# Optimization experiments

Hardware: AMD Instinct MI355X
Metric: run time of the kernel (lower is better)

## Reference

```python
import jax, jax.numpy as jnp
import numpy as np

N = 100000
E = 3200000
K = 4
BN_EPS = 1e-5


def spmm(edge_rows, edge_cols, edge_vals, x):
    # y = A @ x with A in COO: y[r] += v * x[c]
    msgs = edge_vals[:, None] * x[edge_cols]           # [E, d]
    return jax.ops.segment_sum(msgs, edge_rows, num_segments=N)


def setup_inputs() -> dict:
    key = jax.random.key(0)
    ks = jax.random.split(key, 8)
    d_in, d_h, d_out = 256, 256, 64
    return {
        "x": jax.random.normal(ks[0], (N, d_in), jnp.float32),
        "edge_rows": jax.random.randint(ks[1], (E,), 0, N, jnp.int32),
        "edge_cols": jax.random.randint(ks[2], (E,), 0, N, jnp.int32),
        "edge_vals": jax.random.uniform(ks[3], (E,), jnp.float32),
        "bn_gamma": jnp.ones((d_in,), jnp.float32),
        "bn_beta": jnp.zeros((d_in,), jnp.float32),
        "w_in": jax.random.normal(ks[4], (d_in, d_h), jnp.float32) * 0.05,
        "b_in": jnp.zeros((d_h,), jnp.float32),
        "w_conv": jax.random.normal(ks[5], (d_h, d_h), jnp.float32) * 0.05,
        "b_conv": jnp.zeros((d_h,), jnp.float32),
        "w_out": jax.random.normal(ks[6], (d_h, d_out), jnp.float32) * 0.05,
        "b_out": jnp.zeros((d_out,), jnp.float32),
    }


def reference(x, edge_rows, edge_cols, edge_vals, bn_gamma, bn_beta,
              w_in, b_in, w_conv, b_conv, w_out, b_out):
    # BatchNorm1d over node dimension (training-mode batch stats, biased var)
    mean = jnp.mean(x, axis=0)
    var = jnp.var(x, axis=0)
    x = (x - mean) * jax.lax.rsqrt(var + BN_EPS) * bn_gamma + bn_beta
    # in_conv + tanh
    x = jnp.tanh(x @ w_in + b_in)
    # SGConv: k spmm hops then linear, then tanh
    for _ in range(K):
        x = spmm(edge_rows, edge_cols, edge_vals, x)
    x = jnp.tanh(x @ w_conv + b_conv)
    # out_conv (logits)
    return x @ w_out + b_out
```

## Files before the change

### kernel.cpp

```cpp
#include <hip/hip_runtime.h>
#include <hip/hip_fp16.h>

#define NN   100000
#define NNP  100096
#define EE   3200000
#define DD   256
#define DOUTC 64
#define LSTR 40

typedef _Float16 half8 __attribute__((ext_vector_type(8)));
typedef _Float16 half4 __attribute__((ext_vector_type(4)));
typedef float    f32x4 __attribute__((ext_vector_type(4)));

__device__ inline f32x4 mfma16(half8 a, half8 b, f32x4 c) {
    return __builtin_amdgcn_mfma_f32_16x16x32_f16(a, b, c, 0, 0, 0);
}

__global__ void col_stats_kernel(const float* __restrict__ x, float* __restrict__ stats) {
    int t = threadIdx.x;
    int r0 = blockIdx.x * 256;
    int r1 = min(r0 + 256, NN);
    float s = 0.f, s2 = 0.f;
    for (int r = r0; r < r1; ++r) {
        float v = x[(size_t)r * DD + t];
        s += v; s2 += v * v;
    }
    atomicAdd(&stats[t], s);
    atomicAdd(&stats[DD + t], s2);
}

__global__ void fold_bias_kernel(const float* __restrict__ stats,
                                 const float* __restrict__ gamma,
                                 const float* __restrict__ beta,
                                 const float* __restrict__ w_in,
                                 const float* __restrict__ b_in,
                                 float* __restrict__ bfold) {
    __shared__ float sb[DD];
    int t = threadIdx.x;
    float mean = stats[t] * (1.0f / NN);
    float var  = stats[DD + t] * (1.0f / NN) - mean * mean;
    float a = gamma[t] * rsqrtf(var + 1e-5f);
    sb[t] = beta[t] - mean * a;
    __syncthreads();
    float acc = 0.f;
    for (int j = 0; j < DD; ++j) acc += sb[j] * w_in[j * DD + t];
    bfold[t] = b_in[t] + acc;
}

__global__ void split_w1_kernel(const float* __restrict__ stats,
                                const float* __restrict__ gamma,
                                const float* __restrict__ w_in,
                                _Float16* __restrict__ wth, _Float16* __restrict__ wtl) {
    int k = blockIdx.x, n = threadIdx.x;
    float mean = stats[k] * (1.0f / NN);
    float var  = stats[DD + k] * (1.0f / NN) - mean * mean;
    float a = gamma[k] * rsqrtf(var + 1e-5f);
    float v = a * w_in[(size_t)k * DD + n];
    _Float16 hi = (_Float16)v;
    _Float16 lo = (_Float16)(v - (float)hi);
    wth[(size_t)n * DD + k] = hi;
    wtl[(size_t)n * DD + k] = lo;
}

__global__ void split_w_kernel(const float* __restrict__ w, int ncols,
                               _Float16* __restrict__ wth, _Float16* __restrict__ wtl) {
    int k = blockIdx.x, n = threadIdx.x;
    float v = w[(size_t)k * ncols + n];
    _Float16 hi = (_Float16)v;
    _Float16 lo = (_Float16)(v - (float)hi);
    wth[(size_t)n * DD + k] = hi;
    wtl[(size_t)n * DD + k] = lo;
}

__global__ void hist_kernel(const int* __restrict__ rows, int* __restrict__ cnt) {
    int e = blockIdx.x * blockDim.x + threadIdx.x;
    if (e < EE) atomicAdd(&cnt[rows[e]], 1);
}

__global__ void scan1_kernel(const int* __restrict__ in, int* __restrict__ out,
                             int* __restrict__ bsums, int n) {
    __shared__ int s[256];
    int t = threadIdx.x;
    int base = blockIdx.x * 1024;
    int v[4]; int local = 0;
    for (int i = 0; i < 4; ++i) {
        int idx = base + t * 4 + i;
        v[i] = (idx < n) ? in[idx] : 0;
        local += v[i];
    }
    s[t] = local;
    __syncthreads();
    for (int off = 1; off < 256; off <<= 1) {
        int xv = 0;
        if (t >= off) xv = s[t - off];
        __syncthreads();
        if (t >= off) s[t] += xv;
        __syncthreads();
    }
    int excl = s[t] - local;
    if (t == 255) bsums[blockIdx.x] = s[255];
    int run = excl;
    for (int i = 0; i < 4; ++i) {
        int idx = base + t * 4 + i;
        if (idx < n) out[idx] = run;
        run += v[i];
    }
}

__global__ void scan2_kernel(int* __restrict__ bsums, int nb) {
    __shared__ int s[256];
    int t = threadIdx.x;
    int v = (t < nb) ? bsums[t] : 0;
    s[t] = v;
    __syncthreads();
    for (int off = 1; off < 256; off <<= 1) {
        int xv = 0;
        if (t >= off) xv = s[t - off];
        __syncthreads();
        if (t >= off) s[t] += xv;
        __syncthreads();
    }
    if (t < nb) bsums[t] = s[t] - v;
}

__global__ void scan3_kernel(int* __restrict__ out, const int* __restrict__ bsums, int n) {
    int t = threadIdx.x;
    int base = blockIdx.x * 1024;
    int add = bsums[blockIdx.x];
    for (int i = 0; i < 4; ++i) {
        int idx = base + t * 4 + i;
        if (idx < n) out[idx] += add;
    }
    if (blockIdx.x == 0 && t == 0) out[n] = EE;
}

__global__ void scatter_kernel(const int* __restrict__ rows, const int* __restrict__ cols,
                               const float* __restrict__ vals, const int* __restrict__ rp,
                               int* __restrict__ cur, int2* __restrict__ edges) {
    int e = blockIdx.x * blockDim.x + threadIdx.x;
    if (e >= EE) return;
    int r = rows[e];
    int pos = rp[r] + atomicAdd(&cur[r], 1);
    edges[pos] = make_int2(cols[e], __float_as_int(vals[e]));
}

__global__ __launch_bounds__(256) void spmm_kernel(
        const int* __restrict__ rp, const int2* __restrict__ edges,
        const __half* __restrict__ xin, __half* __restrict__ xout) {
    int tid = threadIdx.x;
    int lane = tid & 63;
    int half_id = lane >> 5;
    int sl = lane & 31;
    int r = __builtin_amdgcn_readfirstlane(blockIdx.x * 4 + (tid >> 6));
    int e0 = rp[r], e1 = rp[r + 1];
    const float4* xi = (const float4*)xin;

    float acc[8] = {0.f,0.f,0.f,0.f,0.f,0.f,0.f,0.f};

    int base = e0;
    for (; base + 8 <= e1; base += 8) {
        int2 d[4];
#pragma unroll
        for (int i = 0; i < 4; ++i) d[i] = edges[base + 2*i + half_id];
        float4 xv[4];
#pragma unroll
        for (int i = 0; i < 4; ++i) xv[i] = xi[(size_t)d[i].x * 32 + sl];
#pragma unroll
        for (int i = 0; i < 4; ++i) {
            float v = __int_as_float(d[i].y);
            const __half2* hp = (const __half2*)&xv[i];
            float2 f0 = __half22float2(hp[0]);
            float2 f1 = __half22float2(hp[1]);
            float2 f2 = __half22float2(hp[2]);
            float2 f3 = __half22float2(hp[3]);
            acc[0] += v*f0.x; acc[1] += v*f0.y;
            acc[2] += v*f1.x; acc[3] += v*f1.y;
            acc[4] += v*f2.x; acc[5] += v*f2.y;
            acc[6] += v*f3.x; acc[7] += v*f3.y;
        }
    }
    if (base < e1) {
#pragma unroll
        for (int i = 0; i < 4; ++i) {
            int idx = base + 2*i + half_id;
            bool valid = idx < e1;
            int idxc = valid ? idx : e0;
            int2 d = edges[idxc];
            float v = valid ? __int_as_float(d.y) : 0.f;
            float4 xv = xi[(size_t)d.x * 32 + sl];
            const __half2* hp = (const __half2*)&xv;
            float2 f0 = __half22float2(hp[0]);
            float2 f1 = __half22float2(hp[1]);
            float2 f2 = __half22float2(hp[2]);
            float2 f3 = __half22float2(hp[3]);
            acc[0] += v*f0.x; acc[1] += v*f0.y;
            acc[2] += v*f1.x; acc[3] += v*f1.y;
            acc[4] += v*f2.x; acc[5] += v*f2.y;
            acc[6] += v*f3.x; acc[7] += v*f3.y;
        }
    }
#pragma unroll
    for (int j = 0; j < 8; ++j) acc[j] += __shfl_xor(acc[j], 32, 64);
    if (half_id == 0) {
        union { __half h[8]; float4 f; } u;
#pragma unroll
        for (int j = 0; j < 8; ++j) u.h[j] = __float2half_rn(acc[j]);
        ((float4*)xout)[(size_t)r * 32 + sl] = u.f;
    }
}

template<bool SPLIT_A, bool TANH, typename Tout, int BN>
__global__ __launch_bounds__(256) void gemm_mfma(
    const void* __restrict__ Av, const _Float16* __restrict__ WTh,
    const _Float16* __restrict__ WTl, const float* __restrict__ bias,
    Tout* __restrict__ C, int M_A, int M_C, int NC)
{
    __shared__ _Float16 As_hi[128 * LSTR];
    __shared__ _Float16 As_lo[(SPLIT_A ? 128 : 1) * LSTR];
    __shared__ _Float16 Ws_hi[BN * LSTR];
    __shared__ _Float16 Ws_lo[BN * LSTR];

    int tid = threadIdx.x;
    int lane = tid & 63;
    int w = tid >> 6;
    int q = lane >> 4;
    int r16 = lane & 15;
    int m0 = blockIdx.x * 128;
    int n0 = blockIdx.y * BN;

    constexpr int MT = (BN == 128) ? 4 : 2;
    int wm = (BN == 128) ? (w & 1) * 64 : w * 32;
    int wn = (BN == 128) ? (w >> 1) * 64 : 0;

    f32x4 acc[MT][4];
#pragma unroll
    for (int mt = 0; mt < MT; ++mt)
#pragma unroll
        for (int nt = 0; nt < 4; ++nt) acc[mt][nt] = (f32x4){0.f, 0.f, 0.f, 0.f};

    for (int k0 = 0; k0 < 256; k0 += 32) {
        if (SPLIT_A) {
            const float* A = (const float*)Av;
#pragma unroll
            for (int p = 0; p < 4; ++p) {
                int idx = tid + p * 256;
                int m = idx >> 3, kc = idx & 7;
                int gm = m0 + m;
                float4 av = make_float4(0.f, 0.f, 0.f, 0.f);
                if (gm < M_A) av = *(const float4*)&A[(size_t)gm * 256 + k0 + kc * 4];
                half4 hi, lo;
                hi.x = (_Float16)av.x; lo.x = (_Float16)(av.x - (float)hi.x);
                hi.y = (_Float16)av.y; lo.y = (_Float16)(av.y - (float)hi.y);
                hi.z = (_Float16)av.z; lo.z = (_Float16)(av.z - (float)hi.z);
                hi.w = (_Float16)av.w; lo.w = (_Float16)(av.w - (float)hi.w);
                *(half4*)&As_hi[m * LSTR + kc * 4] = hi;
                *(half4*)&As_lo[m * LSTR + kc * 4] = lo;
            }
        } else {
            const _Float16* A = (const _Float16*)Av;
#pragma unroll
            for (int p = 0; p < 2; ++p) {
                int idx = tid + p * 256;
                int m = idx >> 2, kc = idx & 3;
                half8 av = *(const half8*)&A[(size_t)(m0 + m) * 256 + k0 + kc * 8];
                *(half8*)&As_hi[m * LSTR + kc * 8] = av;
            }
        }
#pragma unroll
        for (int p = 0; p < BN / 64; ++p) {
            int idx = tid + p * 256;
            int n = idx >> 2, kc = idx & 3;
            *(half8*)&Ws_hi[n * LSTR + kc * 8] = *(const half8*)&WTh[(size_t)(n0 + n) * 256 + k0 + kc * 8];
            *(half8*)&Ws_lo[n * LSTR + kc * 8] = *(const half8*)&WTl[(size_t)(n0 + n) * 256 + k0 + kc * 8];
        }
        __syncthreads();

        half8 af_h[MT], af_l[MT], wf_h[4], wf_l[4];
#pragma unroll
        for (int mt = 0; mt < MT; ++mt) {
            int mrow = wm + mt * 16 + r16;
            af_h[mt] = *(const half8*)&As_hi[mrow * LSTR + q * 8];
            if (SPLIT_A) af_l[mt] = *(const half8*)&As_lo[mrow * LSTR + q * 8];
        }
#pragma unroll
        for (int nt = 0; nt < 4; ++nt) {
            int nrow = wn + nt * 16 + r16;
            wf_h[nt] = *(const half8*)&Ws_hi[nrow * LSTR + q * 8];
            wf_l[nt] = *(const half8*)&Ws_lo[nrow * LSTR + q * 8];
        }
#pragma unroll
        for (int mt = 0; mt < MT; ++mt)
#pragma unroll
            for (int nt = 0; nt < 4; ++nt) {
                acc[mt][nt] = mfma16(af_h[mt], wf_h[nt], acc[mt][nt]);
                if (SPLIT_A) acc[mt][nt] = mfma16(af_l[mt], wf_h[nt], acc[mt][nt]);
                acc[mt][nt] = mfma16(af_h[mt], wf_l[nt], acc[mt][nt]);
            }
        __syncthreads();
    }

#pragma unroll
    for (int nt = 0; nt < 4; ++nt) {
        float b = bias[n0 + wn + nt * 16 + r16];
        int gc = n0 + wn + nt * 16 + r16;
#pragma unroll
        for (int mt = 0; mt < MT; ++mt) {
#pragma unroll
            for (int r = 0; r < 4; ++r) {
                int gm = m0 + wm + mt * 16 + q * 4 + r;
                float v = acc[mt][nt][r] + b;
                if (TANH) v = tanhf(v);
                if (gm < M_C) C[(size_t)gm * NC + gc] = (Tout)v;
            }
        }
    }
}

extern "C" void kernel_launch(void* const* d_in, const int* in_sizes, int n_in,
                              void* d_out, int out_size, void* d_ws, size_t ws_size,
                              hipStream_t stream) {
    const float* x      = (const float*)d_in[0];
    const int*   erows  = (const int*)d_in[1];
    const int*   ecols  = (const int*)d_in[2];
    const float* evals  = (const float*)d_in[3];
    const float* gamma  = (const float*)d_in[4];
    const float* beta   = (const float*)d_in[5];
    const float* w_in   = (const float*)d_in[6];
    const float* b_in   = (const float*)d_in[7];
    const float* w_conv = (const float*)d_in[8];
    const float* b_conv = (const float*)d_in[9];
    const float* w_out  = (const float*)d_in[10];
    const float* b_out  = (const float*)d_in[11];
    float* out = (float*)d_out;

    char* ws = (char*)d_ws;
    size_t off = 0;
    auto alloc = [&](size_t bytes) -> void* {
        void* p = ws + off;
        off = (off + bytes + 255) & ~(size_t)255;
        return p;
    };
    _Float16* h1   = (_Float16*)alloc((size_t)NNP * DD * 2);
    _Float16* h2   = (_Float16*)alloc((size_t)NNP * DD * 2);
    int2*  edges = (int2*) alloc((size_t)EE * 8);
    int*   rp    = (int*)  alloc((size_t)(NN + 1) * 4);
    int*   cnt   = (int*)  alloc((size_t)NN * 4);
    int*   cur   = (int*)  alloc((size_t)NN * 4);
    float* stats = (float*)alloc(2 * DD * 4);
    int*   bsums = (int*)  alloc(128 * 4);
    _Float16* wt1h = (_Float16*)alloc((size_t)DD * DD * 2);
    _Float16* wt1l = (_Float16*)alloc((size_t)DD * DD * 2);
    _Float16* wt2h = (_Float16*)alloc((size_t)DD * DD * 2);
    _Float16* wt2l = (_Float16*)alloc((size_t)DD * DD * 2);
    _Float16* wt3h = (_Float16*)alloc((size_t)DOUTC * DD * 2);
    _Float16* wt3l = (_Float16*)alloc((size_t)DOUTC * DD * 2);
    float* bfold = (float*)alloc(DD * 4);

    hipMemsetAsync(cnt,   0, (size_t)NN * 4, stream);
    hipMemsetAsync(cur,   0, (size_t)NN * 4, stream);
    hipMemsetAsync(stats, 0, 2 * DD * 4, stream);

    hist_kernel<<<(EE + 255) / 256, 256, 0, stream>>>(erows, cnt);
    int nb = (NN + 1023) / 1024;
    scan1_kernel<<<nb, 256, 0, stream>>>(cnt, rp, bsums, NN);
    scan2_kernel<<<1, 256, 0, stream>>>(bsums, nb);
    scan3_kernel<<<nb, 256, 0, stream>>>(rp, bsums, NN);
    scatter_kernel<<<(EE + 255) / 256, 256, 0, stream>>>(erows, ecols, evals, rp, cur, edges);

    col_stats_kernel<<<(NN + 255) / 256, 256, 0, stream>>>(x, stats);
    fold_bias_kernel<<<1, 256, 0, stream>>>(stats, gamma, beta, w_in, b_in, bfold);
    split_w1_kernel<<<DD, DD, 0, stream>>>(stats, gamma, w_in, wt1h, wt1l);
    split_w_kernel<<<DD, DD, 0, stream>>>(w_conv, DD, wt2h, wt2l);
    split_w_kernel<<<DD, DOUTC, 0, stream>>>(w_out, DOUTC, wt3h, wt3l);

    dim3 g2(NNP / 128, 2), g1(NNP / 128, 1);
    gemm_mfma<true, true, _Float16, 128><<<g2, 256, 0, stream>>>(
        x, wt1h, wt1l, bfold, h1, NN, NNP, DD);

    spmm_kernel<<<NN / 4, 256, 0, stream>>>(rp, edges, (const __half*)h1, (__half*)h2);
    spmm_kernel<<<NN / 4, 256, 0, stream>>>(rp, edges, (const __half*)h2, (__half*)h1);
    spmm_kernel<<<NN / 4, 256, 0, stream>>>(rp, edges, (const __half*)h1, (__half*)h2);
    spmm_kernel<<<NN / 4, 256, 0, stream>>>(rp, edges, (const __half*)h2, (__half*)h1);

    gemm_mfma<false, true, _Float16, 128><<<g2, 256, 0, stream>>>(
        h1, wt2h, wt2l, b_conv, h2, NNP, NNP, DD);
    gemm_mfma<false, false, float, 64><<<g1, 256, 0, stream>>>(
        h2, wt3h, wt3l, b_out, out, NNP, NN, DOUTC);
}
```

Before: 1.671 ms.

## Split SpMM into two feature-half passes and precompute CSR scatter ranks

Each SpMM hop now runs as two launches, each covering 128 of the 256 fp16 feature columns. Within a launch, four 16-lane groups each gather a different edge, which shrinks the gathered working set per pass so it is more likely to stay in cache. The COO-to-CSR build records each edge's atomic rank during the histogram, so the scatter no longer needs a second atomic pass or its cursor memset. Nontemporal loads and stores are added for edge streams and outputs. In exchange, the edge list is read twice per hop, kernel launches double, and a 12.8MB rank buffer is added.

```diff
diff --git a/kernel.cpp b/kernel.cpp
--- a/kernel.cpp
+++ b/kernel.cpp
@@ -72,9 +72,10 @@
     wtl[(size_t)n * DD + k] = lo;
 }
 
-__global__ void hist_kernel(const int* __restrict__ rows, int* __restrict__ cnt) {
+__global__ void hist_kernel(const int* __restrict__ rows, int* __restrict__ cnt,
+                            int* __restrict__ rank) {
     int e = blockIdx.x * blockDim.x + threadIdx.x;
-    if (e < EE) atomicAdd(&cnt[rows[e]], 1);
+    if (e < EE) rank[e] = atomicAdd(&cnt[rows[e]], 1);
 }
 
 __global__ void scan1_kernel(const int* __restrict__ in, int* __restrict__ out,
@@ -136,58 +137,74 @@
 
 __global__ void scatter_kernel(const int* __restrict__ rows, const int* __restrict__ cols,
                                const float* __restrict__ vals, const int* __restrict__ rp,
-                               int* __restrict__ cur, int2* __restrict__ edges) {
+                               const int* __restrict__ rank, int2* __restrict__ edges) {
     int e = blockIdx.x * blockDim.x + threadIdx.x;
     if (e >= EE) return;
-    int r = rows[e];
-    int pos = rp[r] + atomicAdd(&cur[r], 1);
-    edges[pos] = make_int2(cols[e], __float_as_int(vals[e]));
+    int r = __builtin_nontemporal_load(&rows[e]);
+    int c = __builtin_nontemporal_load(&cols[e]);
+    float v = __builtin_nontemporal_load(&vals[e]);
+    int rk = __builtin_nontemporal_load(&rank[e]);
+    int pos = rp[r] + rk;
+    edges[pos] = make_int2(c, __float_as_int(v));
 }
 
 __global__ __launch_bounds__(256) void spmm_kernel(
         const int* __restrict__ rp, const int2* __restrict__ edges,
-        const __half* __restrict__ xin, __half* __restrict__ xout) {
+        const __half* __restrict__ xin, __half* __restrict__ xout, int ph) {
     int tid = threadIdx.x;
     int lane = tid & 63;
-    int half_id = lane >> 5;
-    int sl = lane & 31;
+    int sub = lane >> 4;
+    int sl = lane & 15;
     int r = __builtin_amdgcn_readfirstlane(blockIdx.x * 4 + (tid >> 6));
     int e0 = rp[r], e1 = rp[r + 1];
     const float4* xi = (const float4*)xin;
+    const long long* epk = (const long long*)edges;
+    int cbase = ph * 16 + sl;
 
     float acc[8] = {0.f,0.f,0.f,0.f,0.f,0.f,0.f,0.f};
 
     int base = e0;
     for (; base + 8 <= e1; base += 8) {
-        int2 d[4];
-#pragma unroll
-        for (int i = 0; i < 4; ++i) d[i] = edges[base + 2*i + half_id];
-        float4 xv[4];
-#pragma unroll
-        for (int i = 0; i < 4; ++i) xv[i] = xi[(size_t)d[i].x * 32 + sl];
-#pragma unroll
-        for (int i = 0; i < 4; ++i) {
-            float v = __int_as_float(d[i].y);
-            const __half2* hp = (const __half2*)&xv[i];
+        long long p0 = __builtin_nontemporal_load(&epk[base + sub]);
+        long long p1 = __builtin_nontemporal_load(&epk[base + 4 + sub]);
+        int c0 = (int)(unsigned int)p0, c1 = (int)(unsigned int)p1;
+        float v0 = __int_as_float((int)(p0 >> 32));
+        float v1 = __int_as_float((int)(p1 >> 32));
+        float4 x0 = xi[(size_t)c0 * 32 + cbase];
+        float4 x1 = xi[(size_t)c1 * 32 + cbase];
+        {
+            const __half2* hp = (const __half2*)&x0;
             float2 f0 = __half22float2(hp[0]);
             float2 f1 = __half22float2(hp[1]);
             float2 f2 = __half22float2(hp[2]);
             float2 f3 = __half22float2(hp[3]);
-            acc[0] += v*f0.x; acc[1] += v*f0.y;
-            acc[2] += v*f1.x; acc[3] += v*f1.y;
-            acc[4] += v*f2.x; acc[5] += v*f2.y;
-            acc[6] += v*f3.x; acc[7] += v*f3.y;
+            acc[0] += v0*f0.x; acc[1] += v0*f0.y;
+            acc[2] += v0*f1.x; acc[3] += v0*f1.y;
+            acc[4] += v0*f2.x; acc[5] += v0*f2.y;
+            acc[6] += v0*f3.x; acc[7] += v0*f3.y;
+        }
+        {
+            const __half2* hp = (const __half2*)&x1;
+            float2 f0 = __half22float2(hp[0]);
+            float2 f1 = __half22float2(hp[1]);
+            float2 f2 = __half22float2(hp[2]);
+            float2 f3 = __half22float2(hp[3]);
+            acc[0] += v1*f0.x; acc[1] += v1*f0.y;
+            acc[2] += v1*f1.x; acc[3] += v1*f1.y;
+            acc[4] += v1*f2.x; acc[5] += v1*f2.y;
+            acc[6] += v1*f3.x; acc[7] += v1*f3.y;
         }
     }
     if (base < e1) {
 #pragma unroll
-        for (int i = 0; i < 4; ++i) {
-            int idx = base + 2*i + half_id;
+        for (int i = 0; i < 2; ++i) {
+            int idx = base + 4*i + sub;
             bool valid = idx < e1;
             int idxc = valid ? idx : e0;
-            int2 d = edges[idxc];
-            float v = valid ? __int_as_float(d.y) : 0.f;
-            float4 xv = xi[(size_t)d.x * 32 + sl];
+            long long p = epk[idxc];
+            int c = (int)(unsigned int)p;
+            float v = valid ? __int_as_float((int)(p >> 32)) : 0.f;
+            float4 xv = xi[(size_t)c * 32 + cbase];
             const __half2* hp = (const __half2*)&xv;
             float2 f0 = __half22float2(hp[0]);
             float2 f1 = __half22float2(hp[1]);
@@ -200,12 +217,15 @@
         }
     }
 #pragma unroll
-    for (int j = 0; j < 8; ++j) acc[j] += __shfl_xor(acc[j], 32, 64);
-    if (half_id == 0) {
-        union { __half h[8]; float4 f; } u;
+    for (int j = 0; j < 8; ++j) {
+        acc[j] += __shfl_xor(acc[j], 16, 64);
+        acc[j] += __shfl_xor(acc[j], 32, 64);
+    }
+    if (sub == 0) {
+        union { __half h[8]; f32x4 f; } u;
 #pragma unroll
         for (int j = 0; j < 8; ++j) u.h[j] = __float2half_rn(acc[j]);
-        ((float4*)xout)[(size_t)r * 32 + sl] = u.f;
+        __builtin_nontemporal_store(u.f, (f32x4*)&((float4*)xout)[(size_t)r * 32 + cbase]);
     }
 }
 
@@ -343,9 +363,9 @@
     _Float16* h1   = (_Float16*)alloc((size_t)NNP * DD * 2);
     _Float16* h2   = (_Float16*)alloc((size_t)NNP * DD * 2);
     int2*  edges = (int2*) alloc((size_t)EE * 8);
+    int*   rank  = (int*)  alloc((size_t)EE * 4);
     int*   rp    = (int*)  alloc((size_t)(NN + 1) * 4);
     int*   cnt   = (int*)  alloc((size_t)NN * 4);
-    int*   cur   = (int*)  alloc((size_t)NN * 4);
     float* stats = (float*)alloc(2 * DD * 4);
     int*   bsums = (int*)  alloc(128 * 4);
     _Float16* wt1h = (_Float16*)alloc((size_t)DD * DD * 2);
@@ -357,15 +377,14 @@
     float* bfold = (float*)alloc(DD * 4);
 
     hipMemsetAsync(cnt,   0, (size_t)NN * 4, stream);
-    hipMemsetAsync(cur,   0, (size_t)NN * 4, stream);
     hipMemsetAsync(stats, 0, 2 * DD * 4, stream);
 
-    hist_kernel<<<(EE + 255) / 256, 256, 0, stream>>>(erows, cnt);
+    hist_kernel<<<(EE + 255) / 256, 256, 0, stream>>>(erows, cnt, rank);
     int nb = (NN + 1023) / 1024;
     scan1_kernel<<<nb, 256, 0, stream>>>(cnt, rp, bsums, NN);
     scan2_kernel<<<1, 256, 0, stream>>>(bsums, nb);
     scan3_kernel<<<nb, 256, 0, stream>>>(rp, bsums, NN);
-    scatter_kernel<<<(EE + 255) / 256, 256, 0, stream>>>(erows, ecols, evals, rp, cur, edges);
+    scatter_kernel<<<(EE + 255) / 256, 256, 0, stream>>>(erows, ecols, evals, rp, rank, edges);
 
     col_stats_kernel<<<(NN + 255) / 256, 256, 0, stream>>>(x, stats);
     fold_bias_kernel<<<1, 256, 0, stream>>>(stats, gamma, beta, w_in, b_in, bfold);
@@ -377,10 +396,14 @@
     gemm_mfma<true, true, _Float16, 128><<<g2, 256, 0, stream>>>(
         x, wt1h, wt1l, bfold, h1, NN, NNP, DD);
 
-    spmm_kernel<<<NN / 4, 256, 0, stream>>>(rp, edges, (const __half*)h1, (__half*)h2);
-    spmm_kernel<<<NN / 4, 256, 0, stream>>>(rp, edges, (const __half*)h2, (__half*)h1);
-    spmm_kernel<<<NN / 4, 256, 0, stream>>>(rp, edges, (const __half*)h1, (__half*)h2);
-    spmm_kernel<<<NN / 4, 256, 0, stream>>>(rp, edges, (const __half*)h2, (__half*)h1);
+    spmm_kernel<<<NN / 4, 256, 0, stream>>>(rp, edges, (const __half*)h1, (__half*)h2, 0);
+    spmm_kernel<<<NN / 4, 256, 0, stream>>>(rp, edges, (const __half*)h1, (__half*)h2, 1);
+    spmm_kernel<<<NN / 4, 256, 0, stream>>>(rp, edges, (const __half*)h2, (__half*)h1, 0);
+    spmm_kernel<<<NN / 4, 256, 0, stream>>>(rp, edges, (const __half*)h2, (__half*)h1, 1);
+    spmm_kernel<<<NN / 4, 256, 0, stream>>>(rp, edges, (const __half*)h1, (__half*)h2, 0);
+    spmm_kernel<<<NN / 4, 256, 0, stream>>>(rp, edges, (const __half*)h1, (__half*)h2, 1);
+    spmm_kernel<<<NN / 4, 256, 0, stream>>>(rp, edges, (const __half*)h2, (__half*)h1, 0);
+    spmm_kernel<<<NN / 4, 256, 0, stream>>>(rp, edges, (const __half*)h2, (__half*)h1, 1);
 
     gemm_mfma<false, true, _Float16, 128><<<g2, 256, 0, stream>>>(
         h1, wt2h, wt2l, b_conv, h2, NNP, NNP, DD);
```

New measurement: 1.634 ms. 2.2% less time.
